# Performance work log

Measured on AMD Instinct MI355X. Metric: run time of the kernel, lower is better.

The kernel has to match this reference:

```python
import jax, jax.numpy as jnp
import numpy as np

N = 100000
E = 1600000
H = 2   # heads
C = 64  # per-head channels
NEG_SLOPE = 0.2


def setup_inputs() -> dict:
    key = jax.random.key(0)
    ks = jax.random.split(key, 12)
    s = 0.05
    return {
        "logits": jax.random.normal(ks[0], (N, 40), jnp.float32),
        "features": jax.random.normal(ks[1], (N, 256), jnp.float32),
        "edge_index": jax.random.randint(ks[2], (2, E), 0, N, jnp.int32),
        "W_feat": jax.random.normal(ks[3], (256, 128), jnp.float32) * s,
        "b_feat": jnp.zeros((128,), jnp.float32),
        "W0": jax.random.normal(ks[4], (168, 128), jnp.float32) * s,
        "att_src0": jax.random.normal(ks[5], (H, C), jnp.float32) * s,
        "att_dst0": jax.random.normal(ks[6], (H, C), jnp.float32) * s,
        "bias0": jnp.zeros((128,), jnp.float32),
        "W1": jax.random.normal(ks[7], (128, 128), jnp.float32) * s,
        "att_src1": jax.random.normal(ks[8], (H, C), jnp.float32) * s,
        "att_dst1": jax.random.normal(ks[9], (H, C), jnp.float32) * s,
        "bias1": jnp.zeros((128,), jnp.float32),
        "W_out": jax.random.normal(ks[10], (128, 40), jnp.float32) * s,
        "b_out": jnp.zeros((40,), jnp.float32),
    }


def gat_conv(x, src, dst, W, att_src, att_dst, bias):
    # x: [N, F_in] -> h: [N, H, C]
    h = (x @ W).reshape(N, H, C)
    a_src = (h * att_src).sum(-1)  # [N, H]
    a_dst = (h * att_dst).sum(-1)  # [N, H]
    # per-edge attention logits, leaky relu
    e = jax.nn.leaky_relu(a_src[src] + a_dst[dst], NEG_SLOPE)  # [E+N, H]
    # segment softmax over incoming edges of each dst node
    e_max = jax.ops.segment_max(e, dst, num_segments=N)
    e_exp = jnp.exp(e - e_max[dst])
    denom = jax.ops.segment_sum(e_exp, dst, num_segments=N)
    alpha = e_exp / (denom[dst] + 1e-16)  # [E+N, H]
    # weighted message aggregation (scatter-add)
    msg = h[src] * alpha[:, :, None]  # [E+N, H, C]
    out = jax.ops.segment_sum(msg, dst, num_segments=N)
    return out.reshape(N, H * C) + bias


def reference(logits, features, edge_index, W_feat, b_feat,
              W0, att_src0, att_dst0, bias0,
              W1, att_src1, att_dst1, bias1,
              W_out, b_out):
    # input assembly: [logits | proj(features)]
    x = jnp.concatenate([logits, features @ W_feat + b_feat], axis=-1)  # [N,168]
    # add self loops (PyG GATConv default add_self_loops=True)
    loops = jnp.arange(N, dtype=edge_index.dtype)
    src = jnp.concatenate([edge_index[0], loops])
    dst = jnp.concatenate([edge_index[1], loops])
    x = gat_conv(x, src, dst, W0, att_src0, att_dst0, bias0)
    x = jax.nn.relu(x)  # relu between conv layers (dropout=0 / eval)
    x = gat_conv(x, src, dst, W1, att_src1, att_dst1, bias1)
    return x @ W_out + b_out  # [N, 40]
```

## Files before the change

### kernel.cpp

```cpp
#include <hip/hip_runtime.h>

#define NN 100000
#define EE 1600000
#define NBUCK ((NN + 255) >> 8)
#define CHUNK 8192
#define NPBLK ((EE + CHUNK - 1) / CHUNK)

typedef __attribute__((ext_vector_type(8))) short short8_t;
typedef __attribute__((ext_vector_type(4))) float f32x4;

static __device__ inline unsigned short f2bf(float f) {
    unsigned int u = __float_as_uint(f);
    u += 0x7FFFu + ((u >> 16) & 1u);
    return (unsigned short)(u >> 16);
}
static __device__ inline float bf2f(unsigned short h) {
    return __uint_as_float(((unsigned int)h) << 16);
}
static __device__ inline float u2f(unsigned int u) { return __uint_as_float(u); }

static __device__ void part_count_body(int bid, int* h, const int* __restrict__ ei,
                                       int* __restrict__ cnt) {
    for (int i = threadIdx.x; i < NBUCK; i += 256) h[i] = 0;
    __syncthreads();
    int e0 = bid * CHUNK;
    int e1 = e0 + CHUNK; if (e1 > EE) e1 = EE;
    for (int e = e0 + threadIdx.x; e < e1; e += 256)
        atomicAdd(&h[ei[EE + e] >> 8], 1);
    __syncthreads();
    for (int i = threadIdx.x; i < NBUCK; i += 256)
        cnt[bid * NBUCK + i] = h[i];
}

static __device__ void part_scan_body(int* S, const int* __restrict__ cnt,
                                      int* __restrict__ base, int* __restrict__ bbase) {
    int* A = S;
    int* B = S + 512;
    int t = threadIdx.x;
    int totLoc[2];
#pragma unroll
    for (int q = 0; q < 2; ++q) {
        int idx = t + q * 256;
        int v = 0;
        if (idx < NBUCK)
            for (int k = 0; k < NPBLK; ++k) v += cnt[k * NBUCK + idx];
        totLoc[q] = v;
        A[idx] = v;
    }
    __syncthreads();
    int* src = A;
    int* dst = B;
    for (int off = 1; off < 512; off <<= 1) {
#pragma unroll
        for (int q = 0; q < 2; ++q) {
            int idx = t + q * 256;
            dst[idx] = src[idx] + (idx >= off ? src[idx - off] : 0);
        }
        __syncthreads();
        int* tmp = src; src = dst; dst = tmp;
    }
#pragma unroll
    for (int q = 0; q < 2; ++q) {
        int idx = t + q * 256;
        if (idx < NBUCK) {
            int excl = src[idx] - totLoc[q];
            bbase[idx] = excl;
            int run = excl;
            for (int k = 0; k < NPBLK; ++k) {
                base[k * NBUCK + idx] = run;
                run += cnt[k * NBUCK + idx];
            }
        }
    }
    if (t == 0) bbase[NBUCK] = EE;
}

static __device__ void part_scatter_body(int bid, int* lcur, const int* __restrict__ ei,
                                         const int* __restrict__ base,
                                         unsigned int* __restrict__ bbuf) {
    for (int i = threadIdx.x; i < NBUCK; i += 256)
        lcur[i] = base[bid * NBUCK + i];
    __syncthreads();
    int e0 = bid * CHUNK;
    int e1 = e0 + CHUNK; if (e1 > EE) e1 = EE;
    for (int e = e0 + threadIdx.x; e < e1; e += 256) {
        int s = ei[e], d = ei[EE + e];
        int pos = atomicAdd(&lcur[d >> 8], 1);
        bbuf[pos] = (unsigned int)s | ((unsigned int)(d & 255) << 24);
    }
}

static __device__ void csr_build_body(int b, int* S, const unsigned int* __restrict__ bbuf,
                                      const int* __restrict__ bbase,
                                      int* __restrict__ row_ptr, int* __restrict__ col) {
    int* hist = S;
    int* sc   = S + 256;
    int* lcur = S + 512;
    int t = threadIdx.x;
    int n0 = b << 8;
    int nCnt = NN - n0; if (nCnt > 256) nCnt = 256;
    int es = bbase[b], ee2 = bbase[b + 1];
    hist[t] = 0;
    __syncthreads();
    for (int i = es + t; i < ee2; i += 256)
        atomicAdd(&hist[bbuf[i] >> 24], 1);
    __syncthreads();
    int v = hist[t];
    sc[t] = v;
    __syncthreads();
    for (int off = 1; off < 256; off <<= 1) {
        int u = (t >= off) ? sc[t - off] : 0;
        __syncthreads();
        sc[t] += u;
        __syncthreads();
    }
    int excl = sc[t] - v;
    if (t < nCnt) row_ptr[n0 + t] = es + excl;
    if (b == 0 && t == 0) row_ptr[NN] = EE;
    lcur[t] = excl;
    __syncthreads();
    for (int i = es + t; i < ee2; i += 256) {
        unsigned int pk = bbuf[i];
        int lpos = atomicAdd(&lcur[pk >> 24], 1);
        col[es + lpos] = (int)(pk & 0x00FFFFFFu);
    }
}

static __device__ void bsplit_body(int col, const float* __restrict__ W, int ldw, int K, int N,
                                   unsigned short* __restrict__ BThi,
                                   unsigned short* __restrict__ BTlo,
                                   int stride, int koff, int KPseg) {
    int k = threadIdx.x;
    if (k >= KPseg) return;
    float v = (k < K && col < N) ? W[(size_t)k * ldw + col] : 0.f;
    unsigned short hi = f2bf(v);
    unsigned short lo = f2bf(v - bf2f(hi));
    BThi[(size_t)col * stride + koff + k] = hi;
    BTlo[(size_t)col * stride + koff + k] = lo;
}

static __device__ void cvec_body(const float* __restrict__ b_feat,
                                 const float* __restrict__ W0, float* __restrict__ cvec) {
    int j = threadIdx.x;
    if (j >= 128) return;
    float s = 0.f;
    for (int k = 0; k < 128; ++k) s += b_feat[k] * W0[(40 + k) * 128 + j];
    cvec[j] = s;
}

template <int OUTBF16, int AMODE, int ATTN, int NCT>
static __device__ void gemm_body(int gbid, unsigned short* lds,
    const void* __restrict__ A1v, int lda1, int K1, int KP1,
    const float* __restrict__ A2, int lda2, int K2,
    int M,
    const unsigned short* __restrict__ BThi, const unsigned short* __restrict__ BTlo,
    int bstride, int KPtot,
    void* __restrict__ Cout, int ldc, int Nact, const float* __restrict__ bias,
    const float* __restrict__ att_src, const float* __restrict__ att_dst,
    float* __restrict__ a_srcO, float* __restrict__ a_dstO)
{
    constexpr int ASZ = (AMODE == 0) ? 4096 : 2048;
    constexpr int BHALF = (NCT == 4) ? 4096 : 2048;
    constexpr int BHI_OFF = ASZ;
    constexpr int BLO_OFF = ASZ + BHALF;

    const int t = threadIdx.x;
    const int w = t >> 6, lane = t & 63;
    const int row0 = gbid * 64;
    const int rbase = (w & 1) * 32;
    const int cbase = (NCT == 4) ? (w >> 1) * 64 : (w >> 1) * 32;

    f32x4 acc[2][NCT];
#pragma unroll
    for (int i = 0; i < 2; ++i)
#pragma unroll
        for (int j = 0; j < NCT; ++j) acc[i][j] = (f32x4){0.f, 0.f, 0.f, 0.f};

    const int arow = t >> 2;
    const int aslot = t & 3;
    const bool rowok = (row0 + arow) < M;
    const int aoff = arow * 32 + (((aslot ^ ((arow >> 1) & 3))) << 3);

    const int bc0 = t >> 2,         bs0 = t & 3;
    const int bc1 = (t + 256) >> 2, bs1 = (t + 256) & 3;
    const int bo0 = bc0 * 32 + ((bs0 ^ ((bc0 >> 1) & 3)) << 3);
    const int bo1 = bc1 * 32 + ((bs1 ^ ((bc1 >> 1) & 3)) << 3);

    float ra[8];
    short8_t rab;
    short8_t rbh0, rbl0, rbh1, rbl1;
    const short8_t zz = {0, 0, 0, 0, 0, 0, 0, 0};

#define LOADB_(k0_) {                                                     \
        size_t g0_ = (size_t)bc0 * bstride + (k0_) + bs0 * 8;             \
        rbh0 = *(const short8_t*)&BThi[g0_];                              \
        rbl0 = *(const short8_t*)&BTlo[g0_];                              \
        if (NCT == 4) {                                                   \
            size_t g1_ = (size_t)bc1 * bstride + (k0_) + bs1 * 8;         \
            rbh1 = *(const short8_t*)&BThi[g1_];                          \
            rbl1 = *(const short8_t*)&BTlo[g1_];                          \
        }                                                                 \
    }

#define LOADA_(k0_) {                                                     \
        if (AMODE == 1) {                                                 \
            int gk = (k0_) + aslot * 8;                                   \
            if (rowok && gk + 8 <= K1) {                                  \
                const unsigned short* Ab =                                \
                    (const unsigned short*)A1v + (size_t)(row0 + arow) * lda1; \
                rab = *(const short8_t*)&Ab[gk];                          \
            } else rab = zz;                                              \
        } else {                                                          \
            const float* Asrc; int gk, Klim;                              \
            if ((k0_) < KP1) {                                            \
                Asrc = (const float*)A1v + (size_t)(row0 + arow) * lda1;  \
                gk = (k0_) + aslot * 8; Klim = K1;                        \
            } else {                                                      \
                Asrc = A2 + (size_t)(row0 + arow) * lda2;                 \
                gk = (k0_) - KP1 + aslot * 8; Klim = K2;                  \
            }                                                             \
            if (rowok && gk + 8 <= Klim) {                                \
                float4 v0 = *(const float4*)(Asrc + gk);                  \
                float4 v1 = *(const float4*)(Asrc + gk + 4);              \
                ra[0] = v0.x; ra[1] = v0.y; ra[2] = v0.z; ra[3] = v0.w;   \
                ra[4] = v1.x; ra[5] = v1.y; ra[6] = v1.z; ra[7] = v1.w;   \
            } else {                                                      \
                for (int j_ = 0; j_ < 8; ++j_) ra[j_] = 0.f;              \
            }                                                             \
        }                                                                 \
    }

    LOADA_(0);
    LOADB_(0);

    for (int k0 = 0; k0 < KPtot; k0 += 32) {
        if (AMODE == 1) {
            *(short8_t*)&lds[aoff] = rab;
        } else if (AMODE == 2) {
            short8_t vh;
#pragma unroll
            for (int j = 0; j < 8; ++j) vh[j] = (short)f2bf(ra[j]);
            *(short8_t*)&lds[aoff] = vh;
        } else {
            short8_t vh, vl;
#pragma unroll
            for (int j = 0; j < 8; ++j) {
                unsigned short hi = f2bf(ra[j]);
                vh[j] = (short)hi;
                vl[j] = (short)f2bf(ra[j] - bf2f(hi));
            }
            *(short8_t*)&lds[aoff] = vh;
            *(short8_t*)&lds[2048 + aoff] = vl;
        }
        *(short8_t*)&lds[BHI_OFF + bo0] = rbh0;
        *(short8_t*)&lds[BLO_OFF + bo0] = rbl0;
        if (NCT == 4) {
            *(short8_t*)&lds[BHI_OFF + bo1] = rbh1;
            *(short8_t*)&lds[BLO_OFF + bo1] = rbl1;
        }
        __syncthreads();

        if (k0 + 32 < KPtot) {
            LOADA_(k0 + 32);
            LOADB_(k0 + 32);
        }

        short8_t Ah[2], Al[2], Bh[NCT], Bl[NCT];
        const int fslot = lane >> 4;
#pragma unroll
        for (int rt = 0; rt < 2; ++rt) {
            int r = rbase + rt * 16 + (lane & 15);
            int off = r * 32 + ((fslot ^ ((r >> 1) & 3)) << 3);
            Ah[rt] = *(const short8_t*)&lds[off];
            if (AMODE == 0) Al[rt] = *(const short8_t*)&lds[2048 + off];
        }
#pragma unroll
        for (int ct = 0; ct < NCT; ++ct) {
            int c = cbase + ct * 16 + (lane & 15);
            int off = c * 32 + ((fslot ^ ((c >> 1) & 3)) << 3);
            Bh[ct] = *(const short8_t*)&lds[BHI_OFF + off];
            Bl[ct] = *(const short8_t*)&lds[BLO_OFF + off];
        }
#pragma unroll
        for (int rt = 0; rt < 2; ++rt)
#pragma unroll
            for (int ct = 0; ct < NCT; ++ct) {
                acc[rt][ct] = __builtin_amdgcn_mfma_f32_16x16x32_bf16(Ah[rt], Bh[ct], acc[rt][ct], 0, 0, 0);
                acc[rt][ct] = __builtin_amdgcn_mfma_f32_16x16x32_bf16(Ah[rt], Bl[ct], acc[rt][ct], 0, 0, 0);
                if (AMODE == 0)
                    acc[rt][ct] = __builtin_amdgcn_mfma_f32_16x16x32_bf16(Al[rt], Bh[ct], acc[rt][ct], 0, 0, 0);
            }
        __syncthreads();
    }

#pragma unroll
    for (int rt = 0; rt < 2; ++rt) {
#pragma unroll
        for (int reg = 0; reg < 4; ++reg) {
            int r = row0 + rbase + rt * 16 + (lane >> 4) * 4 + reg;
            if (ATTN) {
                float ps = 0.f, pd = 0.f;
#pragma unroll
                for (int ct = 0; ct < NCT; ++ct) {
                    int c = cbase + ct * 16 + (lane & 15);
                    ps += acc[rt][ct][reg] * att_src[c];
                    pd += acc[rt][ct][reg] * att_dst[c];
                }
#pragma unroll
                for (int off = 1; off < 16; off <<= 1) {
                    ps += __shfl_xor(ps, off);
                    pd += __shfl_xor(pd, off);
                }
                if (r < M && (lane & 15) == 0) {
                    int head = w >> 1;
                    a_srcO[r * 2 + head] = ps;
                    a_dstO[r * 2 + head] = pd;
                }
            }
            if (r >= M) continue;
#pragma unroll
            for (int ct = 0; ct < NCT; ++ct) {
                int c = cbase + ct * 16 + (lane & 15);
                float v = acc[rt][ct][reg];
                if (OUTBF16) {
                    if (bias) v += bias[c];
                    ((unsigned short*)Cout)[(size_t)r * 128 + c] = f2bf(v);
                } else {
                    if (c < Nact) {
                        if (bias) v += bias[c];
                        ((float*)Cout)[(size_t)r * ldc + c] = v;
                    }
                }
            }
        }
    }
#undef LOADA_
#undef LOADB_
}

__global__ __launch_bounds__(256) void prep1_kernel(
    const int* __restrict__ ei, int* __restrict__ cnt,
    const float* __restrict__ W0, const float* __restrict__ W1,
    const float* __restrict__ W_out, const float* __restrict__ b_feat,
    unsigned short* BT0hi, unsigned short* BT0lo,
    unsigned short* BTbhi, unsigned short* BTblo,
    unsigned short* BT1hi, unsigned short* BT1lo,
    unsigned short* BTohi, unsigned short* BTolo,
    float* __restrict__ cvec)
{
    __shared__ int h[NBUCK];
    int bid = blockIdx.x;
    if (bid < NPBLK) { part_count_body(bid, h, ei, cnt); return; }
    bid -= NPBLK;
    if (bid < 128) { bsplit_body(bid, W0, 128, 40, 128, BT0hi, BT0lo, 320, 0, 64); return; }
    bid -= 128;
    if (bid < 128) { bsplit_body(bid, W0 + 40 * 128, 128, 128, 128, BTbhi, BTblo, 128, 0, 128); return; }
    bid -= 128;
    if (bid < 128) { bsplit_body(bid, W1, 128, 128, 128, BT1hi, BT1lo, 128, 0, 128); return; }
    bid -= 128;
    if (bid < 128) { bsplit_body(bid, W_out, 40, 128, 40, BTohi, BTolo, 128, 0, 128); return; }
    cvec_body(b_feat, W0, cvec);
}

__global__ __launch_bounds__(256) void prep2_kernel(
    const int* __restrict__ cnt, int* __restrict__ pbase, int* __restrict__ bbase,
    const float* __restrict__ W_feat,
    const unsigned short* BTbhi, const unsigned short* BTblo,
    float* __restrict__ Wc)
{
    __shared__ __align__(16) unsigned short smem[12288];
    if (blockIdx.x == 0) {
        part_scan_body((int*)smem, cnt, pbase, bbase);
    } else {
        gemm_body<0, 0, 0, 4>(blockIdx.x - 1, smem,
            W_feat, 128, 128, 128, nullptr, 0, 0, 256,
            BTbhi, BTblo, 128, 128, Wc, 128, 128, nullptr,
            nullptr, nullptr, nullptr, nullptr);
    }
}

__global__ __launch_bounds__(256) void prep3_kernel(
    const int* __restrict__ ei, const int* __restrict__ pbase,
    unsigned int* __restrict__ bbuf,
    const float* __restrict__ Wc,
    unsigned short* BT0hi, unsigned short* BT0lo)
{
    __shared__ int lcur[NBUCK];
    if (blockIdx.x < NPBLK) {
        part_scatter_body(blockIdx.x, lcur, ei, pbase, bbuf);
    } else {
        bsplit_body(blockIdx.x - NPBLK, Wc, 128, 256, 128, BT0hi, BT0lo, 320, 64, 256);
    }
}

__global__ __launch_bounds__(256) void csr_gemm_kernel(
    const unsigned int* __restrict__ bbuf, const int* __restrict__ bbase,
    int* __restrict__ row_ptr, int* __restrict__ colbuf,
    const float* __restrict__ logits, const float* __restrict__ features,
    const unsigned short* BT0hi, const unsigned short* BT0lo,
    unsigned short* __restrict__ hbuf, const float* __restrict__ cvec,
    const float* __restrict__ att_src0, const float* __restrict__ att_dst0,
    float* __restrict__ a_srcb, float* __restrict__ a_dstb)
{
    __shared__ __align__(16) unsigned short smem[10240];
    if (blockIdx.x < NBUCK) {
        csr_build_body(blockIdx.x, (int*)smem, bbuf, bbase, row_ptr, colbuf);
    } else {
        gemm_body<1, 2, 1, 4>(blockIdx.x - NBUCK, smem,
            logits, 40, 40, 64, features, 256, 256, NN,
            BT0hi, BT0lo, 320, 320, hbuf, 128, 128, cvec,
            att_src0, att_dst0, a_srcb, a_dstb);
    }
}

template <int OUTBF16, int AMODE, int ATTN, int NCT>
__global__ __launch_bounds__(256) void gemm_kernel(
    const void* __restrict__ A1v, int lda1, int K1, int KP1,
    const float* __restrict__ A2, int lda2, int K2, int M,
    const unsigned short* __restrict__ BThi, const unsigned short* __restrict__ BTlo,
    int bstride, int KPtot,
    void* __restrict__ Cout, int ldc, int Nact, const float* __restrict__ bias,
    const float* __restrict__ att_src, const float* __restrict__ att_dst,
    float* __restrict__ a_srcO, float* __restrict__ a_dstO)
{
    __shared__ __align__(16) unsigned short lds[((AMODE == 0) ? 4096 : 2048) + ((NCT == 4) ? 8192 : 4096)];
    gemm_body<OUTBF16, AMODE, ATTN, NCT>(blockIdx.x, lds,
        A1v, lda1, K1, KP1, A2, lda2, K2, M, BThi, BTlo, bstride, KPtot,
        Cout, ldc, Nact, bias, att_src, att_dst, a_srcO, a_dstO);
}

template <int RELU, int OUTBF16>
__global__ __launch_bounds__(256) void gat_agg_fused(
    const int* __restrict__ row_ptr, const int* __restrict__ col,
    const float* __restrict__ a_src, const float* __restrict__ a_dst,
    const unsigned short* __restrict__ hb,
    const float* __restrict__ bias, void* __restrict__ out)
{
    int wv = (blockIdx.x * 256 + threadIdx.x) >> 6;
    int lane = threadIdx.x & 63;
    int hl = lane >> 5;
    int l5 = lane & 31;
    int n = wv * 2 + hl;
    if (n >= NN) return;
    int hch = l5 >> 4;
    const uint2* h4 = (const uint2*)hb;

    float2 ad2 = ((const float2*)a_dst)[n];
    float adh = hch ? ad2.y : ad2.x;
    float2 as2 = ((const float2*)a_src)[n];
    float e0 = (hch ? as2.y : as2.x) + adh;
    e0 = e0 > 0.f ? e0 : 0.2f * e0;
    float w = __expf(e0);
    uint2 hv = h4[(size_t)n * 32 + l5];
    float a0 = w * u2f(hv.x << 16);
    float a1 = w * u2f(hv.x & 0xFFFF0000u);
    float a2 = w * u2f(hv.y << 16);
    float a3 = w * u2f(hv.y & 0xFFFF0000u);
    float den = w;

    int rs = row_ptr[n], re = row_ptr[n + 1];
    int deg = re - rs;
    int degO = __shfl(deg, lane ^ 32);
    int degm = deg > degO ? deg : degO;
    int nbm = (degm + 15) >> 4;

    for (int bi = 0; bi < nbm; ++bi) {
        int base = rs + bi * 16;
        int cnt = re - base;
        cnt = cnt < 0 ? 0 : (cnt > 16 ? 16 : cnt);
        int cntO = __shfl(cnt, lane ^ 32);
        int cntm = cnt > cntO ? cnt : cntO;
        int j16 = l5 & 15;
        int sL = 0;
        float wL = 0.f;
        if (j16 < cnt) {
            sL = col[base + j16];
            float2 as = ((const float2*)a_src)[sL];
            float tt = (hch ? as.y : as.x) + adh;
            tt = tt > 0.f ? tt : 0.2f * tt;
            wL = __expf(tt);
        }
        const int sb = hl << 5;
        const int wb = sb + (hch << 4);
        int i = 0;
        for (; i + 8 <= cntm; i += 8) {
            int s[8]; uint2 g[8]; float ws[8];
#pragma unroll
            for (int j = 0; j < 8; ++j) s[j] = __shfl(sL, sb + i + j);
#pragma unroll
            for (int j = 0; j < 8; ++j) g[j] = h4[(size_t)s[j] * 32 + l5];
#pragma unroll
            for (int j = 0; j < 8; ++j) ws[j] = __shfl(wL, wb + i + j);
#pragma unroll
            for (int j = 0; j < 8; ++j) {
                a0 += ws[j] * u2f(g[j].x << 16);
                a1 += ws[j] * u2f(g[j].x & 0xFFFF0000u);
                a2 += ws[j] * u2f(g[j].y << 16);
                a3 += ws[j] * u2f(g[j].y & 0xFFFF0000u);
                den += ws[j];
            }
        }
        for (; i + 4 <= cntm; i += 4) {
            int s[4]; uint2 g[4]; float ws[4];
#pragma unroll
            for (int j = 0; j < 4; ++j) s[j] = __shfl(sL, sb + i + j);
#pragma unroll
            for (int j = 0; j < 4; ++j) g[j] = h4[(size_t)s[j] * 32 + l5];
#pragma unroll
            for (int j = 0; j < 4; ++j) ws[j] = __shfl(wL, wb + i + j);
#pragma unroll
            for (int j = 0; j < 4; ++j) {
                a0 += ws[j] * u2f(g[j].x << 16);
                a1 += ws[j] * u2f(g[j].x & 0xFFFF0000u);
                a2 += ws[j] * u2f(g[j].y << 16);
                a3 += ws[j] * u2f(g[j].y & 0xFFFF0000u);
                den += ws[j];
            }
        }
        for (; i < cntm; ++i) {
            int s = __shfl(sL, sb + i);
            float ws = __shfl(wL, wb + i);
            uint2 g = h4[(size_t)s * 32 + l5];
            a0 += ws * u2f(g.x << 16);
            a1 += ws * u2f(g.x & 0xFFFF0000u);
            a2 += ws * u2f(g.y << 16);
            a3 += ws * u2f(g.y & 0xFFFF0000u);
            den += ws;
        }
    }
    float inv = 1.f / (den + 1e-16f);
    float4 b4 = ((const float4*)bias)[l5];
    float o0 = a0 * inv + b4.x;
    float o1 = a1 * inv + b4.y;
    float o2 = a2 * inv + b4.z;
    float o3 = a3 * inv + b4.w;
    if (RELU) {
        o0 = fmaxf(o0, 0.f); o1 = fmaxf(o1, 0.f);
        o2 = fmaxf(o2, 0.f); o3 = fmaxf(o3, 0.f);
    }
    if (OUTBF16) {
        uint2 pk;
        pk.x = (unsigned int)f2bf(o0) | ((unsigned int)f2bf(o1) << 16);
        pk.y = (unsigned int)f2bf(o2) | ((unsigned int)f2bf(o3) << 16);
        ((uint2*)out)[(size_t)n * 32 + l5] = pk;
    } else {
        ((float4*)out)[(size_t)n * 32 + l5] = make_float4(o0, o1, o2, o3);
    }
}

extern "C" void kernel_launch(void* const* d_in, const int* in_sizes, int n_in,
                              void* d_out, int out_size, void* d_ws, size_t ws_size,
                              hipStream_t stream) {
    const float* logits   = (const float*)d_in[0];
    const float* features = (const float*)d_in[1];
    const int*   ei       = (const int*)d_in[2];
    const float* W_feat   = (const float*)d_in[3];
    const float* b_feat   = (const float*)d_in[4];
    const float* W0       = (const float*)d_in[5];
    const float* att_src0 = (const float*)d_in[6];
    const float* att_dst0 = (const float*)d_in[7];
    const float* bias0    = (const float*)d_in[8];
    const float* W1       = (const float*)d_in[9];
    const float* att_src1 = (const float*)d_in[10];
    const float* att_dst1 = (const float*)d_in[11];
    const float* bias1    = (const float*)d_in[12];
    const float* W_out    = (const float*)d_in[13];
    const float* b_out    = (const float*)d_in[14];
    float* out = (float*)d_out;

    float* agg    = (float*)d_ws;
    float* a_srcb = agg + (size_t)NN * 128;
    float* a_dstb = a_srcb + (size_t)NN * 2;
    float* Wc     = a_dstb + (size_t)NN * 2;
    float* cvec   = Wc + 256 * 128;
    unsigned short* hbuf = (unsigned short*)(cvec + 128);
    unsigned short* BT0hi = hbuf + (size_t)NN * 128;
    unsigned short* BT0lo = BT0hi + 128 * 320;
    unsigned short* BTbhi = BT0lo + 128 * 320;
    unsigned short* BTblo = BTbhi + 128 * 128;
    unsigned short* BT1hi = BTblo + 128 * 128;
    unsigned short* BT1lo = BT1hi + 128 * 128;
    unsigned short* BTohi = BT1lo + 128 * 128;
    unsigned short* BTolo = BTohi + 128 * 128;
    int* row_ptr = (int*)(BTolo + 128 * 128);
    int* colbuf  = row_ptr + NN + 1;
    int* cnt     = colbuf + EE;
    int* pbase   = cnt + NPBLK * NBUCK;
    int* bbase   = pbase + NPBLK * NBUCK;
    unsigned int* bbuf = (unsigned int*)agg;
    unsigned short* aggb = (unsigned short*)agg;

    dim3 blk(256);
    const int gemmGrid = (NN + 63) / 64;
    const int aggGrid = (NN / 2 + 3) / 4;

    prep1_kernel<<<dim3(NPBLK + 4 * 128 + 1), blk, 0, stream>>>(
        ei, cnt, W0, W1, W_out, b_feat,
        BT0hi, BT0lo, BTbhi, BTblo, BT1hi, BT1lo, BTohi, BTolo, cvec);

    prep2_kernel<<<dim3(5), blk, 0, stream>>>(cnt, pbase, bbase, W_feat, BTbhi, BTblo, Wc);

    prep3_kernel<<<dim3(NPBLK + 128), blk, 0, stream>>>(ei, pbase, bbuf, Wc, BT0hi, BT0lo);

    csr_gemm_kernel<<<dim3(NBUCK + gemmGrid), blk, 0, stream>>>(
        bbuf, bbase, row_ptr, colbuf,
        logits, features, BT0hi, BT0lo, hbuf, cvec,
        att_src0, att_dst0, a_srcb, a_dstb);

    gat_agg_fused<1, 1><<<dim3(aggGrid), blk, 0, stream>>>(
        row_ptr, colbuf, a_srcb, a_dstb, hbuf, bias0, aggb);

    gemm_kernel<1, 1, 1, 4><<<dim3(gemmGrid), blk, 0, stream>>>(
        aggb, 128, 128, 128, nullptr, 0, 0, NN,
        BT1hi, BT1lo, 128, 128, hbuf, 128, 128, nullptr,
        att_src1, att_dst1, a_srcb, a_dstb);
    gat_agg_fused<0, 1><<<dim3(aggGrid), blk, 0, stream>>>(
        row_ptr, colbuf, a_srcb, a_dstb, hbuf, bias1, aggb);

    gemm_kernel<0, 1, 0, 2><<<dim3(gemmGrid), blk, 0, stream>>>(
        aggb, 128, 128, 128, nullptr, 0, 0, NN,
        BTohi, BTolo, 128, 128, out, 40, 40, b_out,
        nullptr, nullptr, nullptr, nullptr);
}
```

Baseline: 266.8 us.

## Fuse GAT aggregation with following GEMM via LDS-staged bf16 tile

Merges each gather-aggregate kernel with the next dense GEMM. Each block aggregates 64 destination rows, writes them as bf16 into a swizzled LDS A-tile, then runs the MFMA GEMM against the layer weights. This removes the aggregated-feature round trip through global memory and two kernel launches. The cost is that the gather phase now runs at 64-row block granularity before one barrier, which may reduce latency hiding and occupancy. It also needs separate buffers (hbuf2, a_src1b/a_dst1b) to avoid read/write aliasing.

```diff
diff --git a/kernel.cpp b/kernel.cpp
--- a/kernel.cpp
+++ b/kernel.cpp
@@ -7,6 +7,7 @@
 #define NPBLK ((EE + CHUNK - 1) / CHUNK)
 
 typedef __attribute__((ext_vector_type(8))) short short8_t;
+typedef __attribute__((ext_vector_type(4))) short short4_t;
 typedef __attribute__((ext_vector_type(4))) float f32x4;
 
 static __device__ inline unsigned short f2bf(float f) {
@@ -413,138 +414,248 @@
     }
 }
 
-template <int OUTBF16, int AMODE, int ATTN, int NCT>
-__global__ __launch_bounds__(256) void gemm_kernel(
-    const void* __restrict__ A1v, int lda1, int K1, int KP1,
-    const float* __restrict__ A2, int lda2, int K2, int M,
+template <int RELU, int ATTN, int NCT, int OUTBF16>
+__global__ __launch_bounds__(256) void agg_gemm_kernel(
+    const int* __restrict__ row_ptr, const int* __restrict__ col,
+    const float* __restrict__ a_src, const float* __restrict__ a_dst,
+    const unsigned short* __restrict__ hb, const float* __restrict__ bias,
     const unsigned short* __restrict__ BThi, const unsigned short* __restrict__ BTlo,
-    int bstride, int KPtot,
-    void* __restrict__ Cout, int ldc, int Nact, const float* __restrict__ bias,
+    int bstride,
+    void* __restrict__ Cout, int ldc, int Nact, const float* __restrict__ obias,
     const float* __restrict__ att_src, const float* __restrict__ att_dst,
     float* __restrict__ a_srcO, float* __restrict__ a_dstO)
 {
-    __shared__ __align__(16) unsigned short lds[((AMODE == 0) ? 4096 : 2048) + ((NCT == 4) ? 8192 : 4096)];
-    gemm_body<OUTBF16, AMODE, ATTN, NCT>(blockIdx.x, lds,
-        A1v, lda1, K1, KP1, A2, lda2, K2, M, BThi, BTlo, bstride, KPtot,
-        Cout, ldc, Nact, bias, att_src, att_dst, a_srcO, a_dstO);
-}
-
-template <int RELU, int OUTBF16>
-__global__ __launch_bounds__(256) void gat_agg_fused(
-    const int* __restrict__ row_ptr, const int* __restrict__ col,
-    const float* __restrict__ a_src, const float* __restrict__ a_dst,
-    const unsigned short* __restrict__ hb,
-    const float* __restrict__ bias, void* __restrict__ out)
-{
-    int wv = (blockIdx.x * 256 + threadIdx.x) >> 6;
-    int lane = threadIdx.x & 63;
-    int hl = lane >> 5;
-    int l5 = lane & 31;
-    int n = wv * 2 + hl;
-    if (n >= NN) return;
-    int hch = l5 >> 4;
+    constexpr int ASZ = 8192;
+    constexpr int BHALF = (NCT == 4) ? 4096 : 2048;
+    constexpr int BHI_OFF = ASZ;
+    constexpr int BLO_OFF = ASZ + BHALF;
+    __shared__ __align__(16) unsigned short lds[ASZ + 2 * BHALF];
+
+    const int t = threadIdx.x;
+    const int wv = t >> 6, lane = t & 63;
+    const int hl = lane >> 5;
+    const int l5 = lane & 31;
+    const int hch = l5 >> 4;
+    const int row0 = blockIdx.x * 64;
     const uint2* h4 = (const uint2*)hb;
 
-    float2 ad2 = ((const float2*)a_dst)[n];
-    float adh = hch ? ad2.y : ad2.x;
-    float2 as2 = ((const float2*)a_src)[n];
-    float e0 = (hch ? as2.y : as2.x) + adh;
-    e0 = e0 > 0.f ? e0 : 0.2f * e0;
-    float w = __expf(e0);
-    uint2 hv = h4[(size_t)n * 32 + l5];
-    float a0 = w * u2f(hv.x << 16);
-    float a1 = w * u2f(hv.x & 0xFFFF0000u);
-    float a2 = w * u2f(hv.y << 16);
-    float a3 = w * u2f(hv.y & 0xFFFF0000u);
-    float den = w;
-
-    int rs = row_ptr[n], re = row_ptr[n + 1];
-    int deg = re - rs;
-    int degO = __shfl(deg, lane ^ 32);
-    int degm = deg > degO ? deg : degO;
-    int nbm = (degm + 15) >> 4;
-
-    for (int bi = 0; bi < nbm; ++bi) {
-        int base = rs + bi * 16;
-        int cnt = re - base;
-        cnt = cnt < 0 ? 0 : (cnt > 16 ? 16 : cnt);
-        int cntO = __shfl(cnt, lane ^ 32);
-        int cntm = cnt > cntO ? cnt : cntO;
-        int j16 = l5 & 15;
-        int sL = 0;
-        float wL = 0.f;
-        if (j16 < cnt) {
-            sL = col[base + j16];
-            float2 as = ((const float2*)a_src)[sL];
-            float tt = (hch ? as.y : as.x) + adh;
-            tt = tt > 0.f ? tt : 0.2f * tt;
-            wL = __expf(tt);
-        }
-        const int sb = hl << 5;
-        const int wb = sb + (hch << 4);
-        int i = 0;
-        for (; i + 8 <= cntm; i += 8) {
-            int s[8]; uint2 g[8]; float ws[8];
-#pragma unroll
-            for (int j = 0; j < 8; ++j) s[j] = __shfl(sL, sb + i + j);
-#pragma unroll
-            for (int j = 0; j < 8; ++j) g[j] = h4[(size_t)s[j] * 32 + l5];
-#pragma unroll
-            for (int j = 0; j < 8; ++j) ws[j] = __shfl(wL, wb + i + j);
-#pragma unroll
-            for (int j = 0; j < 8; ++j) {
-                a0 += ws[j] * u2f(g[j].x << 16);
-                a1 += ws[j] * u2f(g[j].x & 0xFFFF0000u);
-                a2 += ws[j] * u2f(g[j].y << 16);
-                a3 += ws[j] * u2f(g[j].y & 0xFFFF0000u);
-                den += ws[j];
-            }
-        }
-        for (; i + 4 <= cntm; i += 4) {
-            int s[4]; uint2 g[4]; float ws[4];
-#pragma unroll
-            for (int j = 0; j < 4; ++j) s[j] = __shfl(sL, sb + i + j);
-#pragma unroll
-            for (int j = 0; j < 4; ++j) g[j] = h4[(size_t)s[j] * 32 + l5];
-#pragma unroll
-            for (int j = 0; j < 4; ++j) ws[j] = __shfl(wL, wb + i + j);
-#pragma unroll
-            for (int j = 0; j < 4; ++j) {
-                a0 += ws[j] * u2f(g[j].x << 16);
-                a1 += ws[j] * u2f(g[j].x & 0xFFFF0000u);
-                a2 += ws[j] * u2f(g[j].y << 16);
-                a3 += ws[j] * u2f(g[j].y & 0xFFFF0000u);
-                den += ws[j];
-            }
-        }
-        for (; i < cntm; ++i) {
-            int s = __shfl(sL, sb + i);
-            float ws = __shfl(wL, wb + i);
-            uint2 g = h4[(size_t)s * 32 + l5];
-            a0 += ws * u2f(g.x << 16);
-            a1 += ws * u2f(g.x & 0xFFFF0000u);
-            a2 += ws * u2f(g.y << 16);
-            a3 += ws * u2f(g.y & 0xFFFF0000u);
-            den += ws;
-        }
-    }
-    float inv = 1.f / (den + 1e-16f);
-    float4 b4 = ((const float4*)bias)[l5];
-    float o0 = a0 * inv + b4.x;
-    float o1 = a1 * inv + b4.y;
-    float o2 = a2 * inv + b4.z;
-    float o3 = a3 * inv + b4.w;
-    if (RELU) {
-        o0 = fmaxf(o0, 0.f); o1 = fmaxf(o1, 0.f);
-        o2 = fmaxf(o2, 0.f); o3 = fmaxf(o3, 0.f);
-    }
-    if (OUTBF16) {
-        uint2 pk;
-        pk.x = (unsigned int)f2bf(o0) | ((unsigned int)f2bf(o1) << 16);
-        pk.y = (unsigned int)f2bf(o2) | ((unsigned int)f2bf(o3) << 16);
-        ((uint2*)out)[(size_t)n * 32 + l5] = pk;
-    } else {
-        ((float4*)out)[(size_t)n * 32 + l5] = make_float4(o0, o1, o2, o3);
+    const int kstepA = l5 >> 3;
+    const int slotA  = (l5 >> 1) & 3;
+    const int halfA  = l5 & 1;
+
+    for (int it = 0; it < 8; ++it) {
+        int r = wv * 16 + it * 2 + hl;
+        int n = row0 + r;
+        bool ok = (n < NN);
+
+        float a0 = 0.f, a1 = 0.f, a2 = 0.f, a3 = 0.f, den = 1.f, adh = 0.f;
+        int rs = 0, re = 0;
+        if (ok) {
+            float2 ad2 = ((const float2*)a_dst)[n];
+            adh = hch ? ad2.y : ad2.x;
+            float2 as2 = ((const float2*)a_src)[n];
+            float e0 = (hch ? as2.y : as2.x) + adh;
+            e0 = e0 > 0.f ? e0 : 0.2f * e0;
+            float w = __expf(e0);
+            uint2 hv = h4[(size_t)n * 32 + l5];
+            a0 = w * u2f(hv.x << 16);
+            a1 = w * u2f(hv.x & 0xFFFF0000u);
+            a2 = w * u2f(hv.y << 16);
+            a3 = w * u2f(hv.y & 0xFFFF0000u);
+            den = w;
+            rs = row_ptr[n];
+            re = row_ptr[n + 1];
+        }
+        int deg = re - rs;
+        int degO = __shfl(deg, lane ^ 32);
+        int degm = deg > degO ? deg : degO;
+        int nbm = (degm + 15) >> 4;
+
+        for (int bi = 0; bi < nbm; ++bi) {
+            int base = rs + bi * 16;
+            int cnt = re - base;
+            cnt = cnt < 0 ? 0 : (cnt > 16 ? 16 : cnt);
+            int cntO = __shfl(cnt, lane ^ 32);
+            int cntm = cnt > cntO ? cnt : cntO;
+            int j16 = l5 & 15;
+            int sL = 0;
+            float wL = 0.f;
+            if (j16 < cnt) {
+                sL = col[base + j16];
+                float2 as = ((const float2*)a_src)[sL];
+                float tt = (hch ? as.y : as.x) + adh;
+                tt = tt > 0.f ? tt : 0.2f * tt;
+                wL = __expf(tt);
+            }
+            const int sb = hl << 5;
+            const int wb = sb + (hch << 4);
+            int i = 0;
+            for (; i + 8 <= cntm; i += 8) {
+                int s[8]; uint2 g[8]; float ws[8];
+#pragma unroll
+                for (int j = 0; j < 8; ++j) s[j] = __shfl(sL, sb + i + j);
+#pragma unroll
+                for (int j = 0; j < 8; ++j) g[j] = h4[(size_t)s[j] * 32 + l5];
+#pragma unroll
+                for (int j = 0; j < 8; ++j) ws[j] = __shfl(wL, wb + i + j);
+#pragma unroll
+                for (int j = 0; j < 8; ++j) {
+                    a0 += ws[j] * u2f(g[j].x << 16);
+                    a1 += ws[j] * u2f(g[j].x & 0xFFFF0000u);
+                    a2 += ws[j] * u2f(g[j].y << 16);
+                    a3 += ws[j] * u2f(g[j].y & 0xFFFF0000u);
+                    den += ws[j];
+                }
+            }
+            for (; i + 4 <= cntm; i += 4) {
+                int s[4]; uint2 g[4]; float ws[4];
+#pragma unroll
+                for (int j = 0; j < 4; ++j) s[j] = __shfl(sL, sb + i + j);
+#pragma unroll
+                for (int j = 0; j < 4; ++j) g[j] = h4[(size_t)s[j] * 32 + l5];
+#pragma unroll
+                for (int j = 0; j < 4; ++j) ws[j] = __shfl(wL, wb + i + j);
+#pragma unroll
+                for (int j = 0; j < 4; ++j) {
+                    a0 += ws[j] * u2f(g[j].x << 16);
+                    a1 += ws[j] * u2f(g[j].x & 0xFFFF0000u);
+                    a2 += ws[j] * u2f(g[j].y << 16);
+                    a3 += ws[j] * u2f(g[j].y & 0xFFFF0000u);
+                    den += ws[j];
+                }
+            }
+            for (; i < cntm; ++i) {
+                int s = __shfl(sL, sb + i);
+                float ws = __shfl(wL, wb + i);
+                uint2 g = h4[(size_t)s * 32 + l5];
+                a0 += ws * u2f(g.x << 16);
+                a1 += ws * u2f(g.x & 0xFFFF0000u);
+                a2 += ws * u2f(g.y << 16);
+                a3 += ws * u2f(g.y & 0xFFFF0000u);
+                den += ws;
+            }
+        }
+        float o0 = 0.f, o1 = 0.f, o2 = 0.f, o3 = 0.f;
+        if (ok) {
+            float inv = 1.f / (den + 1e-16f);
+            float4 b4 = ((const float4*)bias)[l5];
+            o0 = a0 * inv + b4.x;
+            o1 = a1 * inv + b4.y;
+            o2 = a2 * inv + b4.z;
+            o3 = a3 * inv + b4.w;
+            if (RELU) {
+                o0 = fmaxf(o0, 0.f); o1 = fmaxf(o1, 0.f);
+                o2 = fmaxf(o2, 0.f); o3 = fmaxf(o3, 0.f);
+            }
+        }
+        short4_t pk = {(short)f2bf(o0), (short)f2bf(o1), (short)f2bf(o2), (short)f2bf(o3)};
+        int ao = kstepA * 2048 + r * 32 + ((slotA ^ ((r >> 1) & 3)) << 3) + halfA * 4;
+        *(short4_t*)&lds[ao] = pk;
+    }
+    __syncthreads();
+
+    const int rbase = (wv & 1) * 32;
+    const int cbase = (NCT == 4) ? (wv >> 1) * 64 : (wv >> 1) * 32;
+
+    f32x4 acc[2][NCT];
+#pragma unroll
+    for (int i = 0; i < 2; ++i)
+#pragma unroll
+        for (int j = 0; j < NCT; ++j) acc[i][j] = (f32x4){0.f, 0.f, 0.f, 0.f};
+
+    const int bc0 = t >> 2,         bs0 = t & 3;
+    const int bc1 = (t + 256) >> 2, bs1 = (t + 256) & 3;
+    const int bo0 = bc0 * 32 + ((bs0 ^ ((bc0 >> 1) & 3)) << 3);
+    const int bo1 = bc1 * 32 + ((bs1 ^ ((bc1 >> 1) & 3)) << 3);
+
+    short8_t rbh0, rbl0, rbh1, rbl1;
+#define LOADB2_(k0_) {                                                    \
+        size_t g0_ = (size_t)bc0 * bstride + (k0_) + bs0 * 8;             \
+        rbh0 = *(const short8_t*)&BThi[g0_];                              \
+        rbl0 = *(const short8_t*)&BTlo[g0_];                              \
+        if (NCT == 4) {                                                   \
+            size_t g1_ = (size_t)bc1 * bstride + (k0_) + bs1 * 8;         \
+            rbh1 = *(const short8_t*)&BThi[g1_];                          \
+            rbl1 = *(const short8_t*)&BTlo[g1_];                          \
+        }                                                                 \
+    }
+    LOADB2_(0);
+    for (int k0 = 0; k0 < 128; k0 += 32) {
+        *(short8_t*)&lds[BHI_OFF + bo0] = rbh0;
+        *(short8_t*)&lds[BLO_OFF + bo0] = rbl0;
+        if (NCT == 4) {
+            *(short8_t*)&lds[BHI_OFF + bo1] = rbh1;
+            *(short8_t*)&lds[BLO_OFF + bo1] = rbl1;
+        }
+        __syncthreads();
+        if (k0 + 32 < 128) LOADB2_(k0 + 32);
+
+        short8_t Ah[2], Bh[NCT], Bl[NCT];
+        const int fslot = lane >> 4;
+        const int abase = (k0 >> 5) * 2048;
+#pragma unroll
+        for (int rt = 0; rt < 2; ++rt) {
+            int r = rbase + rt * 16 + (lane & 15);
+            Ah[rt] = *(const short8_t*)&lds[abase + r * 32 + ((fslot ^ ((r >> 1) & 3)) << 3)];
+        }
+#pragma unroll
+        for (int ct = 0; ct < NCT; ++ct) {
+            int c = cbase + ct * 16 + (lane & 15);
+            int off = c * 32 + ((fslot ^ ((c >> 1) & 3)) << 3);
+            Bh[ct] = *(const short8_t*)&lds[BHI_OFF + off];
+            Bl[ct] = *(const short8_t*)&lds[BLO_OFF + off];
+        }
+#pragma unroll
+        for (int rt = 0; rt < 2; ++rt)
+#pragma unroll
+            for (int ct = 0; ct < NCT; ++ct) {
+                acc[rt][ct] = __builtin_amdgcn_mfma_f32_16x16x32_bf16(Ah[rt], Bh[ct], acc[rt][ct], 0, 0, 0);
+                acc[rt][ct] = __builtin_amdgcn_mfma_f32_16x16x32_bf16(Ah[rt], Bl[ct], acc[rt][ct], 0, 0, 0);
+            }
+        __syncthreads();
+    }
+#undef LOADB2_
+
+#pragma unroll
+    for (int rt = 0; rt < 2; ++rt) {
+#pragma unroll
+        for (int reg = 0; reg < 4; ++reg) {
+            int r = row0 + rbase + rt * 16 + (lane >> 4) * 4 + reg;
+            if (ATTN) {
+                float ps = 0.f, pd = 0.f;
+#pragma unroll
+                for (int ct = 0; ct < NCT; ++ct) {
+                    int c = cbase + ct * 16 + (lane & 15);
+                    ps += acc[rt][ct][reg] * att_src[c];
+                    pd += acc[rt][ct][reg] * att_dst[c];
+                }
+#pragma unroll
+                for (int off = 1; off < 16; off <<= 1) {
+                    ps += __shfl_xor(ps, off);
+                    pd += __shfl_xor(pd, off);
+                }
+                if (r < NN && (lane & 15) == 0) {
+                    int head = wv >> 1;
+                    a_srcO[r * 2 + head] = ps;
+                    a_dstO[r * 2 + head] = pd;
+                }
+            }
+            if (r >= NN) continue;
+#pragma unroll
+            for (int ct = 0; ct < NCT; ++ct) {
+                int c = cbase + ct * 16 + (lane & 15);
+                float v = acc[rt][ct][reg];
+                if (OUTBF16) {
+                    if (obias) v += obias[c];
+                    ((unsigned short*)Cout)[(size_t)r * 128 + c] = f2bf(v);
+                } else {
+                    if (c < Nact) {
+                        if (obias) v += obias[c];
+                        ((float*)Cout)[(size_t)r * ldc + c] = v;
+                    }
+                }
+            }
+        }
     }
 }
 
@@ -568,8 +679,8 @@
     const float* b_out    = (const float*)d_in[14];
     float* out = (float*)d_out;
 
-    float* agg    = (float*)d_ws;
-    float* a_srcb = agg + (size_t)NN * 128;
+    float* reg0   = (float*)d_ws;
+    float* a_srcb = reg0 + (size_t)NN * 128;
     float* a_dstb = a_srcb + (size_t)NN * 2;
     float* Wc     = a_dstb + (size_t)NN * 2;
     float* cvec   = Wc + 256 * 128;
@@ -587,12 +698,13 @@
     int* cnt     = colbuf + EE;
     int* pbase   = cnt + NPBLK * NBUCK;
     int* bbase   = pbase + NPBLK * NBUCK;
-    unsigned int* bbuf = (unsigned int*)agg;
-    unsigned short* aggb = (unsigned short*)agg;
+    float* a_src1b = (float*)(bbase + NBUCK + 1);
+    float* a_dst1b = a_src1b + (size_t)NN * 2;
+    unsigned int* bbuf = (unsigned int*)reg0;
+    unsigned short* hbuf2 = (unsigned short*)reg0;
 
     dim3 blk(256);
     const int gemmGrid = (NN + 63) / 64;
-    const int aggGrid = (NN / 2 + 3) / 4;
 
     prep1_kernel<<<dim3(NPBLK + 4 * 128 + 1), blk, 0, stream>>>(
         ei, cnt, W0, W1, W_out, b_feat,
@@ -607,18 +719,15 @@
         logits, features, BT0hi, BT0lo, hbuf, cvec,
         att_src0, att_dst0, a_srcb, a_dstb);
 
-    gat_agg_fused<1, 1><<<dim3(aggGrid), blk, 0, stream>>>(
-        row_ptr, colbuf, a_srcb, a_dstb, hbuf, bias0, aggb);
-
-    gemm_kernel<1, 1, 1, 4><<<dim3(gemmGrid), blk, 0, stream>>>(
-        aggb, 128, 128, 128, nullptr, 0, 0, NN,
-        BT1hi, BT1lo, 128, 128, hbuf, 128, 128, nullptr,
-        att_src1, att_dst1, a_srcb, a_dstb);
-    gat_agg_fused<0, 1><<<dim3(aggGrid), blk, 0, stream>>>(
-        row_ptr, colbuf, a_srcb, a_dstb, hbuf, bias1, aggb);
-
-    gemm_kernel<0, 1, 0, 2><<<dim3(gemmGrid), blk, 0, stream>>>(
-        aggb, 128, 128, 128, nullptr, 0, 0, NN,
-        BTohi, BTolo, 128, 128, out, 40, 40, b_out,
+    agg_gemm_kernel<1, 1, 4, 1><<<dim3(gemmGrid), blk, 0, stream>>>(
+        row_ptr, colbuf, a_srcb, a_dstb, hbuf, bias0,
+        BT1hi, BT1lo, 128,
+        hbuf2, 128, 128, nullptr,
+        att_src1, att_dst1, a_src1b, a_dst1b);
+
+    agg_gemm_kernel<0, 0, 2, 0><<<dim3(gemmGrid), blk, 0, stream>>>(
+        row_ptr, colbuf, a_src1b, a_dst1b, hbuf2, bias1,
+        BTohi, BTolo, 128,
+        out, 40, 40, b_out,
         nullptr, nullptr, nullptr, nullptr);
 }
```

New measurement: 289.9 us. +8.6%, slower.
